# Optimization experiments

Hardware: AMD Instinct MI355X
Metric: run time of the kernel (lower is better)

## Reference

```python
import jax, jax.numpy as jnp
import numpy as np

N = 100000
E = 1600000
IN_C, HID_C, OUT_C = 128, 64, 64
LAYERS = 2


def setup_inputs() -> dict:
    key = jax.random.key(0)
    ks = jax.random.split(key, 7)
    x = jax.random.normal(ks[0], (N, IN_C), dtype=jnp.float32)
    edge_index = jax.random.randint(ks[1], (2, E), 0, N, dtype=jnp.int32)
    W_init = jax.random.normal(ks[2], (IN_C, HID_C), dtype=jnp.float32) / np.sqrt(IN_C)
    W_self = jax.random.normal(ks[3], (LAYERS, HID_C, HID_C), dtype=jnp.float32) / np.sqrt(HID_C)
    W_agg = jax.random.normal(ks[4], (LAYERS, HID_C, HID_C), dtype=jnp.float32) / np.sqrt(HID_C)
    b = jnp.zeros((LAYERS, HID_C), dtype=jnp.float32)
    W_out = jax.random.normal(ks[5], (HID_C, OUT_C), dtype=jnp.float32) / np.sqrt(HID_C)
    return {"x": x, "edge_index": edge_index, "W_init": W_init,
            "W_self": W_self, "W_agg": W_agg, "b": b, "W_out": W_out}


def reference(x, edge_index, W_init, W_self, W_agg, b, W_out):
    # edge (dst, src): aggregated_neighbors[edge[0]].append(x[edge[1]])
    dst = edge_index[0]
    src = edge_index[1]
    n = x.shape[0]
    # in-degree for mean aggregation (clamp to 1 for isolated nodes)
    deg = jax.ops.segment_sum(jnp.ones((src.shape[0],), dtype=x.dtype), dst,
                              num_segments=n)
    deg = jnp.maximum(deg, 1.0)[:, None]  # [N,1]
    h = x @ W_init  # initialize: [N, hid]
    for l in range(LAYERS):
        msgs = h[src]  # per-edge gather [E, hid]
        agg = jax.ops.segment_sum(msgs, dst, num_segments=n) / deg  # mean aggregate
        h = jax.nn.relu(agg @ W_agg[l] + h @ W_self[l] + b[l])  # combine
    return h @ W_out  # output: [N, out]
```

## Files before the change

### kernel.cpp

```cpp
#include <hip/hip_runtime.h>
#include <hip/hip_fp16.h>

#define N_NODES 100000
#define E_EDGES 1600000
#define IN_C    128
#define HID_C   64
#define OUT_C   64
#define ROWS    32
#define NBUCK   391
#define BSHIFT  8
#define BNODES  256
#define CAP     5120
#define CHUNK   4096
#define NB_BINCH 391
#define NB_TR   112
#define IDXCAP  1632
#define IDXMAX  1568

typedef _Float16 f16x8 __attribute__((ext_vector_type(8)));
typedef float    f32x4 __attribute__((ext_vector_type(4)));
#define MFMA16(a, b, c) __builtin_amdgcn_mfma_f32_16x16x32_f16(a, b, c, 0, 0, 0)

struct BinS {
    int hist[NBUCK]; int resbase[NBUCK]; int cur[NBUCK];
    unsigned pk[CHUNK]; unsigned short bk[CHUNK];
};

__global__ __launch_bounds__(256) void k1_bin_tr(const int* __restrict__ ei,
                                                 int* __restrict__ bucket_cursor,
                                                 unsigned* __restrict__ gbuck,
                                                 const float* __restrict__ Wi,
                                                 const float* __restrict__ Wsf,
                                                 const float* __restrict__ Waf,
                                                 const float* __restrict__ Wo,
                                                 _Float16* __restrict__ wtr) {
    __shared__ BinS S;
    int tid = threadIdx.x;
    if (blockIdx.x < NB_BINCH) {
        for (int i = tid; i < NBUCK; i += 256) S.hist[i] = 0;
        __syncthreads();
        int base = blockIdx.x * CHUNK;
        for (int i = tid; i < CHUNK; i += 256) {
            int e = base + i;
            if (e < E_EDGES) {
                int dst = ei[e];
                int src = ei[E_EDGES + e];
                int b = dst >> BSHIFT;
                S.pk[i] = ((unsigned)(dst & (BNODES - 1)) << 17) | (unsigned)src;
                S.bk[i] = (unsigned short)b;
                atomicAdd(&S.hist[b], 1);
            } else S.bk[i] = 0xFFFF;
        }
        __syncthreads();
        for (int i = tid; i < NBUCK; i += 256) {
            S.resbase[i] = atomicAdd(&bucket_cursor[i], S.hist[i]);
            S.cur[i] = 0;
        }
        __syncthreads();
        for (int i = tid; i < CHUNK; i += 256) {
            if (S.bk[i] != 0xFFFF) {
                int b = S.bk[i];
                int slot = S.resbase[b] + atomicAdd(&S.cur[b], 1);
                if (slot < CAP) gbuck[(size_t)b * CAP + slot] = S.pk[i];
            }
        }
    } else {
        int t = (blockIdx.x - NB_BINCH) * 256 + tid;
        if (t < 8192) {
            int k = t >> 6, col = t & 63;
            wtr[col * 136 + k] = (_Float16)Wi[t];
        } else if (t < 24576) {
            int u = t - 8192; int l = u >> 13; int v = u & 8191;
            int k = v >> 6, col = v & 63;
            float w = (k < 64) ? Waf[l * 4096 + k * 64 + col] : Wsf[l * 4096 + (k - 64) * 64 + col];
            wtr[8704 + l * 8704 + col * 136 + k] = (_Float16)w;
        } else if (t < 28672) {
            int u = t - 24576; int k = u >> 6, col = u & 63;
            wtr[26112 + col * 72 + k] = (_Float16)Wo[u];
        }
    }
}

struct InitS { _Float16 sA[ROWS][IN_C + 8]; _Float16 sBt[HID_C][IN_C + 8]; };
struct BuildS { int lcnt[BNODES]; int lpos[BNODES]; int lcur[BNODES]; int s[2][512]; };
union K2S { InitS ini; BuildS bld; };

template<int K>
__device__ __forceinline__ void mfma_tile(const _Float16* sA, const _Float16* sBt,
                                          int lane, int wave, f32x4 acc[2]) {
    const int LDA = K + 8;
    int r0 = (wave >> 1) * 16;
    int wc = wave & 1;
    int m = lane & 15, kg = lane >> 4;
    acc[0] = (f32x4){0.f, 0.f, 0.f, 0.f};
    acc[1] = (f32x4){0.f, 0.f, 0.f, 0.f};
    #pragma unroll
    for (int ks = 0; ks < K / 32; ++ks) {
        f16x8 a = *(const f16x8*)&sA[(r0 + m) * LDA + 32 * ks + 8 * kg];
        #pragma unroll
        for (int nt = 0; nt < 2; ++nt) {
            f16x8 b = *(const f16x8*)&sBt[(wc * 32 + nt * 16 + m) * LDA + 32 * ks + 8 * kg];
            acc[nt] = MFMA16(a, b, acc[nt]);
        }
    }
}

template<int NKS>
__device__ __forceinline__ void mfma_regB(const _Float16* aBase, int lda, int m,
                                          int kg, const f16x8* bf0, const f16x8* bf1,
                                          f32x4 acc[2]) {
    #pragma unroll
    for (int ks = 0; ks < NKS; ++ks) {
        f16x8 a = *(const f16x8*)&aBase[m * lda + 32 * ks + 8 * kg];
        acc[0] = MFMA16(a, bf0[ks], acc[0]);
        acc[1] = MFMA16(a, bf1[ks], acc[1]);
    }
}

__global__ __launch_bounds__(256) void k2_build_init(const unsigned* __restrict__ gbuck,
                                                     const int* __restrict__ bucket_cursor,
                                                     int* __restrict__ csr,
                                                     int2* __restrict__ rc,
                                                     const float* __restrict__ x,
                                                     const float4* __restrict__ wtrI,
                                                     __half* __restrict__ h) {
    __shared__ K2S U;
    int t = threadIdx.x;
    if (blockIdx.x < NBUCK) {
        BuildS& S = U.bld;
        int b = blockIdx.x;
        int v0 = (t < NBUCK) ? min(bucket_cursor[t], CAP) : 0;
        int v1 = (t + 256 < NBUCK) ? min(bucket_cursor[t + 256], CAP) : 0;
        S.s[0][t] = v0; S.s[0][t + 256] = v1;
        S.lcnt[t] = 0; S.lcur[t] = 0;
        __syncthreads();
        int p = 0;
        for (int off = 1; off < 512; off <<= 1) {
            int a0 = S.s[p][t]       + ((t >= off)       ? S.s[p][t - off] : 0);
            int a1 = S.s[p][t + 256] + ((t + 256 >= off) ? S.s[p][t + 256 - off] : 0);
            S.s[p ^ 1][t] = a0; S.s[p ^ 1][t + 256] = a1;
            __syncthreads();
            p ^= 1;
        }
        int bb = (b == 0) ? 0 : S.s[p][b - 1];
        int ec = min(bucket_cursor[b], CAP);
        int gnode = b * BNODES;
        int nn = min(BNODES, N_NODES - gnode);
        const unsigned* mybuck = gbuck + (size_t)b * CAP;
        __syncthreads();
        for (int i = t; i < ec; i += 256) atomicAdd(&S.lcnt[mybuck[i] >> 17], 1);
        __syncthreads();
        int c = S.lcnt[t];
        S.s[0][t] = c;
        __syncthreads();
        int q = 0;
        for (int off = 1; off < 256; off <<= 1) {
            int a0 = S.s[q][t] + ((t >= off) ? S.s[q][t - off] : 0);
            S.s[q ^ 1][t] = a0;
            __syncthreads();
            q ^= 1;
        }
        int ex = S.s[q][t] - c;
        S.lpos[t] = ex;
        if (t < nn) rc[gnode + t] = make_int2(bb + ex, c);
        __syncthreads();
        for (int i = t; i < ec; i += 256) {
            unsigned pkt = mybuck[i];
            int dl = pkt >> 17;
            int slot = S.lpos[dl] + atomicAdd(&S.lcur[dl], 1);
            csr[bb + slot] = (int)(pkt & 0x1FFFF);
        }
    } else {
        InitS& S = U.ini;
        int row0 = (blockIdx.x - NBUCK) * ROWS;
        float4* sB4 = (float4*)&S.sBt[0][0];
        for (int i = t; i < 1088; i += 256) sB4[i] = wtrI[i];
        const float4* x4 = (const float4*)x;
        for (int i = t; i < ROWS * 32; i += 256) {
            int r = i >> 5, qq = i & 31;
            float4 f = x4[(size_t)(row0 + r) * 32 + qq];
            __half2 ha = __floats2half2_rn(f.x, f.y), hb = __floats2half2_rn(f.z, f.w);
            uint2 u; u.x = *(unsigned*)&ha; u.y = *(unsigned*)&hb;
            *(uint2*)&S.sA[r][qq * 4] = u;
        }
        __syncthreads();
        int lane = t & 63, wave = t >> 6;
        f32x4 acc[2];
        mfma_tile<IN_C>(&S.sA[0][0], &S.sBt[0][0], lane, wave, acc);
        int m = lane & 15, rg = lane >> 4;
        int r0 = (wave >> 1) * 16, wc = wave & 1;
        #pragma unroll
        for (int nt = 0; nt < 2; ++nt) {
            int col = wc * 32 + nt * 16 + m;
            #pragma unroll
            for (int i = 0; i < 4; ++i) {
                int row = row0 + r0 + rg * 4 + i;
                h[(size_t)row * HID_C + col] = __float2half(acc[nt][i]);
            }
        }
    }
}

template<bool FINAL>
__global__ __launch_bounds__(256, 8) void fused_layer(const __half* __restrict__ h,
                                                      const int2* __restrict__ rc,
                                                      const int* __restrict__ csr,
                                                      const _Float16* __restrict__ wB,
                                                      const float* __restrict__ bias,
                                                      __half* __restrict__ hout,
                                                      const _Float16* __restrict__ wO,
                                                      float* __restrict__ out) {
    __shared__ _Float16 sA[ROWS][136];
    __shared__ int sIdx[IDXCAP];
    __shared__ int2 sRC[ROWS];
    int tid = threadIdx.x;
    int wave = tid >> 6, lane = tid & 63;
    int m = lane & 15, kg = lane >> 4, wc = wave & 1;
    int row0 = blockIdx.x * ROWS;
    const uint4* h4 = (const uint4*)h;

    if (tid < 32) sRC[tid] = rc[row0 + tid];
    int2 rcF = rc[row0];
    int2 rcL = rc[row0 + 31];
    int e0 = __builtin_amdgcn_readfirstlane(rcF.x);
    int e1 = __builtin_amdgcn_readfirstlane(rcL.x) + __builtin_amdgcn_readfirstlane(rcL.y);
    int Lc = min(e1 - e0, IDXMAX);
    for (int i = tid; i < Lc; i += 256) sIdx[i] = csr[e0 + i];
    if (tid < 64) sIdx[min(Lc + tid, IDXCAP - 1)] = 0;
    {
        int r = tid >> 3, qq = tid & 7;
        *(uint4*)&sA[r][64 + qq * 8] = h4[(size_t)(row0 + r) * 8 + qq];
    }
    __syncthreads();

    int e8  = lane >> 3;
    int c8l = lane & 7;
    int sl[8], dd[8];
    int dmax = 0;
    #pragma unroll
    for (int r = 0; r < 8; ++r) {
        int2 v = sRC[wave * 8 + r];
        sl[r] = min(__builtin_amdgcn_readfirstlane(v.x) - e0, IDXMAX);
        dd[r] = __builtin_amdgcn_readfirstlane(v.y);
        dmax = max(dmax, dd[r]);
    }
    const __half2 hzero = __floats2half2_rn(0.f, 0.f);
    __half2 p[8][4];
    #pragma unroll
    for (int r = 0; r < 8; ++r) {
        #pragma unroll
        for (int tctr = 0; tctr < 4; ++tctr) p[r][tctr] = hzero;
    }

    for (int c8 = 0; c8 < dmax; c8 += 8) {
        #pragma unroll
        for (int r = 0; r < 8; ++r) {
            if (c8 < dd[r]) {
                int ee = c8 + e8;
                int src = sIdx[sl[r] + ee];
                uint4 vv = h4[(size_t)src * 8 + c8l];
                bool ok = ee < dd[r];
                unsigned w0 = ok ? vv.x : 0u, w1 = ok ? vv.y : 0u;
                unsigned w2 = ok ? vv.z : 0u, w3 = ok ? vv.w : 0u;
                p[r][0] += *(__half2*)&w0;
                p[r][1] += *(__half2*)&w1;
                p[r][2] += *(__half2*)&w2;
                p[r][3] += *(__half2*)&w3;
            }
        }
    }

    #pragma unroll
    for (int r = 0; r < 8; ++r) {
        #pragma unroll
        for (int tctr = 0; tctr < 4; ++tctr) {
            unsigned u = *(unsigned*)&p[r][tctr];
            unsigned o8  = (unsigned)__shfl_xor((int)u, 8);
            p[r][tctr] += *(__half2*)&o8;
            u = *(unsigned*)&p[r][tctr];
            unsigned o16 = (unsigned)__shfl_xor((int)u, 16);
            p[r][tctr] += *(__half2*)&o16;
            u = *(unsigned*)&p[r][tctr];
            unsigned o32 = (unsigned)__shfl_xor((int)u, 32);
            p[r][tctr] += *(__half2*)&o32;
        }
        if (lane < 8) {
            __half2 hinv = __float2half2_rn(1.f / fmaxf((float)dd[r], 1.f));
            __half2 q0 = p[r][0] * hinv, q1 = p[r][1] * hinv;
            __half2 q2 = p[r][2] * hinv, q3 = p[r][3] * hinv;
            uint4 o;
            o.x = *(unsigned*)&q0; o.y = *(unsigned*)&q1;
            o.z = *(unsigned*)&q2; o.w = *(unsigned*)&q3;
            *(uint4*)&sA[wave * 8 + r][8 * lane] = o;
        }
    }

    f16x8 bf0[4], bf1[4];
    #pragma unroll
    for (int ks = 0; ks < 4; ++ks) {
        bf0[ks] = *(const f16x8*)&wB[(wc * 32 + m) * 136 + 32 * ks + 8 * kg];
        bf1[ks] = *(const f16x8*)&wB[(wc * 32 + 16 + m) * 136 + 32 * ks + 8 * kg];
    }
    __syncthreads();

    f32x4 acc[2];
    acc[0] = (f32x4){0.f, 0.f, 0.f, 0.f};
    acc[1] = (f32x4){0.f, 0.f, 0.f, 0.f};
    int r0 = (wave >> 1) * 16;
    mfma_regB<4>(&sA[r0][0], 136, m, kg, bf0, bf1, acc);
    int rg = lane >> 4;
    if (!FINAL) {
        #pragma unroll
        for (int nt = 0; nt < 2; ++nt) {
            int col = wc * 32 + nt * 16 + m;
            float bv = bias[col];
            f32x4 a = (nt == 0) ? acc[0] : acc[1];
            #pragma unroll
            for (int i = 0; i < 4; ++i) {
                int row = row0 + r0 + rg * 4 + i;
                hout[(size_t)row * HID_C + col] = __float2half(fmaxf(a[i] + bv, 0.f));
            }
        }
    } else {
        __syncthreads();
        _Float16* sA72 = &sA[0][0];
        #pragma unroll
        for (int nt = 0; nt < 2; ++nt) {
            int col = wc * 32 + nt * 16 + m;
            float bv = bias[col];
            f32x4 a = (nt == 0) ? acc[0] : acc[1];
            #pragma unroll
            for (int i = 0; i < 4; ++i) {
                int rl = r0 + rg * 4 + i;
                sA72[rl * 72 + col] = (_Float16)fmaxf(a[i] + bv, 0.f);
            }
        }
        f16x8 of0[2], of1[2];
        #pragma unroll
        for (int ks = 0; ks < 2; ++ks) {
            of0[ks] = *(const f16x8*)&wO[(wc * 32 + m) * 72 + 32 * ks + 8 * kg];
            of1[ks] = *(const f16x8*)&wO[(wc * 32 + 16 + m) * 72 + 32 * ks + 8 * kg];
        }
        __syncthreads();
        f32x4 acc2[2];
        acc2[0] = (f32x4){0.f, 0.f, 0.f, 0.f};
        acc2[1] = (f32x4){0.f, 0.f, 0.f, 0.f};
        mfma_regB<2>(&sA72[r0 * 72], 72, m, kg, of0, of1, acc2);
        #pragma unroll
        for (int nt = 0; nt < 2; ++nt) {
            int col = wc * 32 + nt * 16 + m;
            f32x4 a = (nt == 0) ? acc2[0] : acc2[1];
            #pragma unroll
            for (int i = 0; i < 4; ++i) {
                int row = row0 + r0 + rg * 4 + i;
                out[(size_t)row * OUT_C + col] = a[i];
            }
        }
    }
}

extern "C" void kernel_launch(void* const* d_in, const int* in_sizes, int n_in,
                              void* d_out, int out_size, void* d_ws, size_t ws_size,
                              hipStream_t stream) {
    const float* x      = (const float*)d_in[0];
    const int*   ei     = (const int*)  d_in[1];
    const float* W_init = (const float*)d_in[2];
    const float* W_self = (const float*)d_in[3];
    const float* W_agg  = (const float*)d_in[4];
    const float* b      = (const float*)d_in[5];
    const float* W_out  = (const float*)d_in[6];
    float* out = (float*)d_out;

    char* ws = (char*)d_ws;
    const size_t KB = 1 << 10;
    int*      bucket_cursor = (int*)(ws + 0);
    int2*     rc            = (int2*)(ws + 4 * KB);
    int*      csr           = (int*)(ws + 1024 * KB);
    _Float16* wtr           = (_Float16*)(ws + 7424 * KB);
    unsigned* gbuck         = (unsigned*)(ws + 8192 * KB);
    __half*   hA            = (__half*)(ws + 18432 * KB);
    __half*   hB            = (__half*)(ws + 32768 * KB);

    const float4*   wtrI  = (const float4*)(wtr);
    const _Float16* wtrL0 = wtr + 8704;
    const _Float16* wtrL1 = wtr + 17408;
    const _Float16* wtrO  = wtr + 26112;

    hipMemsetAsync(bucket_cursor, 0, NBUCK * sizeof(int), stream);
    k1_bin_tr<<<NB_BINCH + NB_TR, 256, 0, stream>>>(ei, bucket_cursor, gbuck,
                                                    W_init, W_self, W_agg, W_out, wtr);
    k2_build_init<<<NBUCK + N_NODES / ROWS, 256, 0, stream>>>(gbuck, bucket_cursor, csr, rc,
                                                              x, wtrI, hA);
    const int GB = N_NODES / ROWS;
    fused_layer<false><<<GB, 256, 0, stream>>>(hA, rc, csr, wtrL0, b + 0 * HID_C, hB,
                                               wtrO, out);
    fused_layer<true><<<GB, 256, 0, stream>>>(hB, rc, csr, wtrL1, b + 1 * HID_C, hA,
                                              wtrO, out);
}
```

Baseline: 142.6 us.

## Split layer-0 aggregation into per-plane gathers over a channel-planar feature copy

The init kernel also writes the hidden features in a planar layout of four 16-channel planes. Layer 0's fused gather-plus-GEMM kernel is replaced by two kernels: a gather that works on one plane at a time, and a separate MFMA combine kernel. Each gather pass reads a much smaller array, so random neighbour reads should hit in L2 more often. In exchange it adds an extra planar write, an intermediate aggregate round trip and one more launch, and it reads the CSR indices four times.

Result: slower. 191.5 us (+34.3%).

```diff
diff --git a/kernel.cpp b/kernel.cpp
--- a/kernel.cpp
+++ b/kernel.cpp
@@ -16,6 +16,8 @@
 #define NB_TR   112
 #define IDXCAP  1632
 #define IDXMAX  1568
+#define PLANES  4
+#define PCH     16
 
 typedef _Float16 f16x8 __attribute__((ext_vector_type(8)));
 typedef float    f32x4 __attribute__((ext_vector_type(4)));
@@ -123,7 +125,8 @@
                                                      int2* __restrict__ rc,
                                                      const float* __restrict__ x,
                                                      const float4* __restrict__ wtrI,
-                                                     __half* __restrict__ h) {
+                                                     __half* __restrict__ h,
+                                                     __half* __restrict__ hP) {
     __shared__ K2S U;
     int t = threadIdx.x;
     if (blockIdx.x < NBUCK) {
@@ -192,11 +195,133 @@
         #pragma unroll
         for (int nt = 0; nt < 2; ++nt) {
             int col = wc * 32 + nt * 16 + m;
+            int plane = wc * 2 + nt;
+            f32x4 a = (nt == 0) ? acc[0] : acc[1];
             #pragma unroll
             for (int i = 0; i < 4; ++i) {
                 int row = row0 + r0 + rg * 4 + i;
-                h[(size_t)row * HID_C + col] = __float2half(acc[nt][i]);
-            }
+                __half hv = __float2half(a[i]);
+                h[(size_t)row * HID_C + col] = hv;
+                hP[((size_t)plane * N_NODES + row) * PCH + m] = hv;
+            }
+        }
+    }
+}
+
+__global__ __launch_bounds__(256, 8) void plane_gather(const __half* __restrict__ hP,
+                                                       const int2* __restrict__ rc,
+                                                       const int* __restrict__ csr,
+                                                       __half* __restrict__ agg) {
+    __shared__ int sIdx[IDXCAP];
+    __shared__ int2 sRC[ROWS];
+    int tid = threadIdx.x;
+    int bid = blockIdx.x;
+    int plane = bid & 3;
+    int row0 = (bid >> 2) * ROWS;
+    if (tid < 32) sRC[tid] = rc[row0 + tid];
+    int2 rcF = rc[row0];
+    int2 rcL = rc[row0 + 31];
+    int e0 = __builtin_amdgcn_readfirstlane(rcF.x);
+    int e1 = __builtin_amdgcn_readfirstlane(rcL.x) + __builtin_amdgcn_readfirstlane(rcL.y);
+    int Lc = min(e1 - e0, IDXMAX);
+    for (int i = tid; i < Lc; i += 256) sIdx[i] = __builtin_nontemporal_load(&csr[e0 + i]);
+    if (tid < 64) sIdx[min(Lc + tid, IDXCAP - 1)] = 0;
+    __syncthreads();
+
+    int wave = tid >> 6, lane = tid & 63;
+    int e16 = lane >> 2;
+    int c4  = lane & 3;
+    const uint2* hp2 = (const uint2*)(hP + (size_t)plane * N_NODES * PCH);
+    int sl[8], dd[8];
+    int dmax = 0;
+    #pragma unroll
+    for (int r = 0; r < 8; ++r) {
+        int2 v = sRC[wave * 8 + r];
+        sl[r] = min(__builtin_amdgcn_readfirstlane(v.x) - e0, IDXMAX);
+        dd[r] = __builtin_amdgcn_readfirstlane(v.y);
+        dmax = max(dmax, dd[r]);
+    }
+    const __half2 hz = __floats2half2_rn(0.f, 0.f);
+    __half2 p0[8], p1[8];
+    #pragma unroll
+    for (int r = 0; r < 8; ++r) { p0[r] = hz; p1[r] = hz; }
+
+    for (int c16 = 0; c16 < dmax; c16 += 16) {
+        #pragma unroll
+        for (int r = 0; r < 8; ++r) {
+            if (c16 < dd[r]) {
+                int ee = c16 + e16;
+                int src = sIdx[sl[r] + ee];
+                uint2 vv = hp2[(size_t)src * 4 + c4];
+                bool ok = ee < dd[r];
+                unsigned w0 = ok ? vv.x : 0u, w1 = ok ? vv.y : 0u;
+                p0[r] += *(__half2*)&w0;
+                p1[r] += *(__half2*)&w1;
+            }
+        }
+    }
+
+    #pragma unroll
+    for (int r = 0; r < 8; ++r) {
+        #pragma unroll
+        for (int off = 4; off <= 32; off <<= 1) {
+            unsigned u0 = *(unsigned*)&p0[r];
+            unsigned o0 = (unsigned)__shfl_xor((int)u0, off);
+            p0[r] += *(__half2*)&o0;
+            unsigned u1 = *(unsigned*)&p1[r];
+            unsigned o1 = (unsigned)__shfl_xor((int)u1, off);
+            p1[r] += *(__half2*)&o1;
+        }
+        if (lane < 4) {
+            __half2 hinv = __float2half2_rn(1.f / fmaxf((float)dd[r], 1.f));
+            __half2 q0 = p0[r] * hinv, q1 = p1[r] * hinv;
+            unsigned long long w = (unsigned long long)(*(unsigned*)&q0)
+                                 | ((unsigned long long)(*(unsigned*)&q1) << 32);
+            __builtin_nontemporal_store(w, (unsigned long long*)
+                &agg[(size_t)(row0 + wave * 8 + r) * HID_C + plane * PCH + lane * 4]);
+        }
+    }
+}
+
+__global__ __launch_bounds__(256, 4) void combine_rows(const __half* __restrict__ aggT,
+                                                       const __half* __restrict__ hSelf,
+                                                       const _Float16* __restrict__ wB,
+                                                       const float* __restrict__ bias,
+                                                       __half* __restrict__ hout) {
+    __shared__ _Float16 sA[ROWS][136];
+    int tid = threadIdx.x;
+    int row0 = blockIdx.x * ROWS;
+    const uint4* a4 = (const uint4*)aggT;
+    const uint4* h4 = (const uint4*)hSelf;
+    {
+        int r = tid >> 3, q = tid & 7;
+        *(uint4*)&sA[r][q * 8]      = a4[(size_t)(row0 + r) * 8 + q];
+        *(uint4*)&sA[r][64 + q * 8] = h4[(size_t)(row0 + r) * 8 + q];
+    }
+    int wave = tid >> 6, lane = tid & 63;
+    int m = lane & 15, kg = lane >> 4, wc = wave & 1;
+    f16x8 bf0[4], bf1[4];
+    #pragma unroll
+    for (int ks = 0; ks < 4; ++ks) {
+        bf0[ks] = *(const f16x8*)&wB[(wc * 32 + m) * 136 + 32 * ks + 8 * kg];
+        bf1[ks] = *(const f16x8*)&wB[(wc * 32 + 16 + m) * 136 + 32 * ks + 8 * kg];
+    }
+    __syncthreads();
+    f32x4 acc[2];
+    acc[0] = (f32x4){0.f, 0.f, 0.f, 0.f};
+    acc[1] = (f32x4){0.f, 0.f, 0.f, 0.f};
+    int r0 = (wave >> 1) * 16;
+    mfma_regB<4>(&sA[r0][0], 136, m, kg, bf0, bf1, acc);
+    int rg = lane >> 4;
+    #pragma unroll
+    for (int nt = 0; nt < 2; ++nt) {
+        int col = wc * 32 + nt * 16 + m;
+        float bv = bias[col];
+        f32x4 a = (nt == 0) ? acc[0] : acc[1];
+        #pragma unroll
+        for (int i = 0; i < 4; ++i) {
+            int row = row0 + r0 + rg * 4 + i;
+            hout[(size_t)row * HID_C + col] = __float2half(fmaxf(a[i] + bv, 0.f));
         }
     }
 }
@@ -251,7 +376,6 @@
         #pragma unroll
         for (int tctr = 0; tctr < 4; ++tctr) p[r][tctr] = hzero;
     }
-
     for (int c8 = 0; c8 < dmax; c8 += 8) {
         #pragma unroll
         for (int r = 0; r < 8; ++r) {
@@ -269,7 +393,6 @@
             }
         }
     }
-
     #pragma unroll
     for (int r = 0; r < 8; ++r) {
         #pragma unroll
@@ -294,7 +417,6 @@
             *(uint4*)&sA[wave * 8 + r][8 * lane] = o;
         }
     }
-
     f16x8 bf0[4], bf1[4];
     #pragma unroll
     for (int ks = 0; ks < 4; ++ks) {
@@ -377,9 +499,11 @@
     int2*     rc            = (int2*)(ws + 4 * KB);
     int*      csr           = (int*)(ws + 1024 * KB);
     _Float16* wtr           = (_Float16*)(ws + 7424 * KB);
-    unsigned* gbuck         = (unsigned*)(ws + 8192 * KB);
-    __half*   hA            = (__half*)(ws + 18432 * KB);
-    __half*   hB            = (__half*)(ws + 32768 * KB);
+    __half*   hA            = (__half*)(ws + 7552 * KB);
+    __half*   hAp           = (__half*)(ws + 20480 * KB);
+    __half*   hB            = (__half*)(ws + 20480 * KB);
+    unsigned* gbuck         = (unsigned*)(ws + 33280 * KB);
+    __half*   agg           = (__half*)(ws + 33280 * KB);
 
     const float4*   wtrI  = (const float4*)(wtr);
     const _Float16* wtrL0 = wtr + 8704;
@@ -390,10 +514,12 @@
     k1_bin_tr<<<NB_BINCH + NB_TR, 256, 0, stream>>>(ei, bucket_cursor, gbuck,
                                                     W_init, W_self, W_agg, W_out, wtr);
     k2_build_init<<<NBUCK + N_NODES / ROWS, 256, 0, stream>>>(gbuck, bucket_cursor, csr, rc,
-                                                              x, wtrI, hA);
+                                                              x, wtrI, hA, hAp);
     const int GB = N_NODES / ROWS;
-    fused_layer<false><<<GB, 256, 0, stream>>>(hA, rc, csr, wtrL0, b + 0 * HID_C, hB,
-                                               wtrO, out);
+
+    plane_gather<<<GB * PLANES, 256, 0, stream>>>(hAp, rc, csr, agg);
+    combine_rows<<<GB, 256, 0, stream>>>(agg, hA, wtrL0, b + 0 * HID_C, hB);
+
     fused_layer<true><<<GB, 256, 0, stream>>>(hB, rc, csr, wtrL1, b + 1 * HID_C, hA,
                                               wtrO, out);
 }
```
